# Performance work log

Hardware: AMD Instinct MI355X
Metric: run time of the kernel (lower is better)

Reference implementation:

```python
import jax, jax.numpy as jnp
import numpy as np

D_MODEL = 1024
N_HEAD = 16
B, S = 4, 2048


def setup_inputs() -> dict:
    key = jax.random.key(0)
    ks = jax.random.split(key, 13)
    s = 1.0 / np.sqrt(D_MODEL)
    inp = {
        "query": jax.random.normal(ks[0], (B, S, D_MODEL), jnp.float32),
        "key_": jax.random.normal(ks[1], (B, S, D_MODEL), jnp.float32),
        "value": jax.random.normal(ks[2], (B, S, D_MODEL), jnp.float32),
        "mask": jax.random.randint(ks[3], (B, 1, S, S), 0, 2, jnp.int32),
        "Wq": jax.random.normal(ks[4], (D_MODEL, D_MODEL), jnp.float32) * s,
        "bq": jax.random.normal(ks[5], (D_MODEL,), jnp.float32) * 0.02,
        "Wk": jax.random.normal(ks[6], (D_MODEL, D_MODEL), jnp.float32) * s,
        "bk": jax.random.normal(ks[7], (D_MODEL,), jnp.float32) * 0.02,
        "Wv": jax.random.normal(ks[8], (D_MODEL, D_MODEL), jnp.float32) * s,
        "bv": jax.random.normal(ks[9], (D_MODEL,), jnp.float32) * 0.02,
        "Wo": jax.random.normal(ks[10], (D_MODEL, D_MODEL), jnp.float32) * s,
        "bo": jax.random.normal(ks[11], (D_MODEL,), jnp.float32) * 0.02,
    }
    return inp


def _split_heads(x):
    b, l, d = x.shape
    return x.reshape(b, l, N_HEAD, d // N_HEAD).transpose(0, 2, 1, 3)  # [B,H,S,Dh]


def reference(query, key_, value, mask, Wq, bq, Wk, bk, Wv, bv, Wo, bo):
    q = _split_heads(query @ Wq + bq)
    k = _split_heads(key_ @ Wk + bk)
    v = _split_heads(value @ Wv + bv)
    dh = q.shape[-1]
    score = jnp.einsum("bhqd,bhkd->bhqk", q, k) / jnp.sqrt(jnp.float32(dh))
    score = jnp.where(mask == 0, jnp.float32(-1e9), score)
    attn = jax.nn.softmax(score, axis=-1)
    out = jnp.einsum("bhqk,bhkd->bhqd", attn, v)  # [B,H,S,Dh]
    b, h, l, d = out.shape
    out = out.transpose(0, 2, 1, 3).reshape(b, l, h * d)
    return out @ Wo + bo
```

## Files before the change

### kernel.cpp

```cpp
#include <hip/hip_runtime.h>
#include <hip/hip_bf16.h>
#include <stdint.h>

#define D_MODEL 1024
#define NHEAD   16
#define DH      64
#define BATCH   4
#define SEQ     2048

typedef __bf16 bf16;
typedef __bf16 bf16x8 __attribute__((ext_vector_type(8)));
typedef __bf16 bf16x4 __attribute__((ext_vector_type(4)));
typedef float  f32x4  __attribute__((ext_vector_type(4)));

#define QSCALE 0.180336876f
#define MFIX   24.0f

__device__ __forceinline__ void gload16(const void* g, void* l) {
    __builtin_amdgcn_global_load_lds((const __attribute__((address_space(1))) uint32_t*)g,
                                     (__attribute__((address_space(3))) uint32_t*)l, 16, 0, 0);
}

__global__ __launch_bounds__(256) void wt4_kernel(const float* __restrict__ W0,
                                                  const float* __restrict__ W1,
                                                  const float* __restrict__ W2,
                                                  const float* __restrict__ W3,
                                                  bf16* __restrict__ Wt3,
                                                  bf16* __restrict__ WtO) {
    __shared__ float t[32][33];
    int z = blockIdx.z;
    const float* W = z == 0 ? W0 : (z == 1 ? W1 : (z == 2 ? W2 : W3));
    bf16* Wt = z < 3 ? Wt3 + (long long)z * (1024ll * 1024) : WtO;
    int x = threadIdx.x, y = threadIdx.y;
    int bi = blockIdx.x * 32;
    int bj = blockIdx.y * 32;
#pragma unroll
    for (int j = 0; j < 4; ++j)
        t[y + j * 8][x] = W[(bi + y + j * 8) * D_MODEL + bj + x];
    __syncthreads();
#pragma unroll
    for (int j = 0; j < 4; ++j)
        Wt[(long long)(bj + y + j * 8) * D_MODEL + bi + x] = (bf16)t[x][y + j * 8];
}

__global__ __launch_bounds__(256) void f2b3_kernel(const float* __restrict__ q,
                                                   const float* __restrict__ k,
                                                   const float* __restrict__ v,
                                                   bf16* __restrict__ out) {
    int third = blockIdx.x >> 12;
    int wi = blockIdx.x & 4095;
    const float* in = third == 0 ? q : (third == 1 ? k : v);
    long long i = (long long)wi * 2048 + threadIdx.x * 8;
    float4 a = *(const float4*)&in[i];
    float4 b = *(const float4*)&in[i + 4];
    bf16x8 o;
    o[0] = (bf16)a.x; o[1] = (bf16)a.y; o[2] = (bf16)a.z; o[3] = (bf16)a.w;
    o[4] = (bf16)b.x; o[5] = (bf16)b.y; o[6] = (bf16)b.z; o[7] = (bf16)b.w;
    *(bf16x8*)&out[(long long)third * (8192ll * 1024) + i] = o;
}

__global__ __launch_bounds__(256) void maskpack_kernel(const int* __restrict__ mask,
                                                       unsigned* __restrict__ bits) {
    long long tid = (long long)blockIdx.x * 256 + threadIdx.x;
    int lane = threadIdx.x & 63;
    long long wid = tid >> 6;
    int m = mask[wid * 64 + lane];
    unsigned long long bal = __ballot(m != 0);
    if (lane == 0) *(unsigned long long*)&bits[wid * 2] = bal;
}

__global__ __launch_bounds__(256) void gemm_qkv_kernel(const bf16* __restrict__ A3,
                                                       const bf16* __restrict__ Wt3,
                                                       const float* __restrict__ bq,
                                                       const float* __restrict__ bk,
                                                       const float* __restrict__ bv,
                                                       bf16* __restrict__ out3) {
    constexpr int K = D_MODEL;
    __shared__ bf16 As[2][128][32];
    __shared__ bf16 Bs[2][128][32];
    int tid = threadIdx.x;
    int l = tid & 63, w = tid >> 6;
    int g = l >> 4, c = l & 15;
    int wm = (w >> 1) * 64, wn = (w & 1) * 64;
    int third = blockIdx.y >> 6;
    long long m0 = (long long)(blockIdx.y & 63) * 128;
    int n0 = blockIdx.x * 128;
    const bf16* A  = A3  + (long long)third * (8192ll * 1024);
    const bf16* Bt = Wt3 + (long long)third * (1024ll * 1024);
    const float* bias = third == 0 ? bq : (third == 1 ? bk : bv);
    float osc = third == 0 ? QSCALE : 1.0f;
    bf16* C = out3 + (long long)third * (8192ll * 1024);
    int srow = l >> 2, scolb = (l & 3) * 16;

    f32x4 acc[4][4] = {};

    for (int k0 = 0; k0 < K; k0 += 64) {
#pragma unroll
        for (int kk = 0; kk < 2; ++kk)
#pragma unroll
            for (int i = 0; i < 2; ++i) {
                int ck = w * 2 + i;
                int row = ck * 16 + srow;
                gload16((const char*)(A + (m0 + row) * K + k0 + kk * 32) + scolb,
                        (char*)&As[kk][0][0] + ck * 1024);
                gload16((const char*)(Bt + (long long)(n0 + row) * K + k0 + kk * 32) + scolb,
                        (char*)&Bs[kk][0][0] + ck * 1024);
            }
        __syncthreads();
#pragma unroll
        for (int kk = 0; kk < 2; ++kk) {
            bf16x8 af[4], bfr[4];
#pragma unroll
            for (int i = 0; i < 4; ++i) af[i] = *(const bf16x8*)&As[kk][wm + i * 16 + c][g * 8];
#pragma unroll
            for (int i = 0; i < 4; ++i) bfr[i] = *(const bf16x8*)&Bs[kk][wn + i * 16 + c][g * 8];
#pragma unroll
            for (int mi = 0; mi < 4; ++mi)
#pragma unroll
                for (int ni = 0; ni < 4; ++ni)
                    acc[mi][ni] = __builtin_amdgcn_mfma_f32_16x16x32_bf16(af[mi], bfr[ni],
                                                                         acc[mi][ni], 0, 0, 0);
        }
        __syncthreads();
    }

#pragma unroll
    for (int mi = 0; mi < 4; ++mi) {
#pragma unroll
        for (int ni = 0; ni < 4; ++ni) {
            int n = n0 + wn + ni * 16 + c;
            float bv_ = bias[n];
            int h = n >> 6, f = n & 63;
#pragma unroll
            for (int r = 0; r < 4; ++r) {
                long long m = m0 + wm + mi * 16 + g * 4 + r;
                float val = (acc[mi][ni][r] + bv_) * osc;
                int b = (int)(m >> 11), s = (int)(m & 2047);
                C[((long long)(b * NHEAD + h) * SEQ + s) * DH + f] = (bf16)val;
            }
        }
    }
}

__global__ __launch_bounds__(256) void gemm_out_kernel(const bf16* __restrict__ A,
                                                       const bf16* __restrict__ Bt,
                                                       const float* __restrict__ bias,
                                                       float* __restrict__ Cptr) {
    constexpr int K = D_MODEL;
    __shared__ bf16 As[2][128][32];
    __shared__ bf16 Bs[2][128][32];
    int tid = threadIdx.x;
    int l = tid & 63, w = tid >> 6;
    int g = l >> 4, c = l & 15;
    int wm = (w >> 1) * 64, wn = (w & 1) * 64;
    long long m0 = (long long)blockIdx.y * 128;
    int n0 = blockIdx.x * 128;
    int srow = l >> 2, scolb = (l & 3) * 16;

    f32x4 acc[4][4] = {};

    for (int k0 = 0; k0 < K; k0 += 64) {
#pragma unroll
        for (int kk = 0; kk < 2; ++kk)
#pragma unroll
            for (int i = 0; i < 2; ++i) {
                int ck = w * 2 + i;
                int row = ck * 16 + srow;
                gload16((const char*)(A + (m0 + row) * K + k0 + kk * 32) + scolb,
                        (char*)&As[kk][0][0] + ck * 1024);
                gload16((const char*)(Bt + (long long)(n0 + row) * K + k0 + kk * 32) + scolb,
                        (char*)&Bs[kk][0][0] + ck * 1024);
            }
        __syncthreads();
#pragma unroll
        for (int kk = 0; kk < 2; ++kk) {
            bf16x8 af[4], bfr[4];
#pragma unroll
            for (int i = 0; i < 4; ++i) af[i] = *(const bf16x8*)&As[kk][wm + i * 16 + c][g * 8];
#pragma unroll
            for (int i = 0; i < 4; ++i) bfr[i] = *(const bf16x8*)&Bs[kk][wn + i * 16 + c][g * 8];
#pragma unroll
            for (int mi = 0; mi < 4; ++mi)
#pragma unroll
                for (int ni = 0; ni < 4; ++ni)
                    acc[mi][ni] = __builtin_amdgcn_mfma_f32_16x16x32_bf16(af[mi], bfr[ni],
                                                                         acc[mi][ni], 0, 0, 0);
        }
        __syncthreads();
    }

#pragma unroll
    for (int mi = 0; mi < 4; ++mi)
#pragma unroll
        for (int ni = 0; ni < 4; ++ni) {
            int n = n0 + wn + ni * 16 + c;
            float bv = bias[n];
#pragma unroll
            for (int r = 0; r < 4; ++r) {
                long long m = m0 + wm + mi * 16 + g * 4 + r;
                Cptr[m * D_MODEL + n] = acc[mi][ni][r] + bv;
            }
        }
}

__global__ __launch_bounds__(256) void vtrans_kernel(const bf16* __restrict__ in,
                                                     bf16* __restrict__ out) {
    __shared__ bf16 t[64][72];
    int bh = blockIdx.y;
    int s0 = blockIdx.x * 64;
    int tid = threadIdx.x;
#pragma unroll
    for (int i = 0; i < 2; ++i) {
        int ck = tid + i * 256;
        int s = ck >> 3, f0 = (ck & 7) * 8;
        bf16x8 v = *(const bf16x8*)&in[((long long)bh * SEQ + s0 + s) * DH + f0];
#pragma unroll
        for (int j = 0; j < 8; ++j) t[f0 + j][s] = v[j];
    }
    __syncthreads();
#pragma unroll
    for (int i = 0; i < 2; ++i) {
        int ck = tid + i * 256;
        int f = ck >> 3, c0 = (ck & 7) * 8;
        bf16x8 v = *(const bf16x8*)&t[f][c0];
        *(bf16x8*)&out[((long long)bh * DH + f) * SEQ + s0 + c0] = v;
    }
}

__global__ __launch_bounds__(512) void attn_kernel(const bf16* __restrict__ Q,
                                                   const bf16* __restrict__ Kt,
                                                   const bf16* __restrict__ Vt,
                                                   const unsigned* __restrict__ bits,
                                                   bf16* __restrict__ O) {
    __shared__ bf16 Ks[2][64][64];
    __shared__ bf16 Vs[2][64][64];
    __shared__ bf16 Ps[8][16][64];
    int tid = threadIdx.x;
    int l = tid & 63, w = tid >> 6;
    int g = l >> 4, c = l & 15;
    int orig = blockIdx.x;
    int swz = (orig & 7) * 128 + (orig >> 3);
    int bh = swz >> 4, qb = swz & 15;
    int b = bh >> 4, h = bh & 15;
    int q0 = qb * 128;
    int q = q0 + w * 16 + c;

    const long long kbase = (long long)bh * SEQ * DH;
    const long long vbase = (long long)bh * DH * SEQ;

    bf16x8 qf0, qf1;
    {
        long long base = ((long long)bh * SEQ + q) * DH + g * 8;
        qf0 = *(const bf16x8*)&Q[base];
        qf1 = *(const bf16x8*)&Q[base + 32];
    }

    int row = tid >> 3;
    int scolb = ((tid & 7) ^ (row & 7)) * 16;

    f32x4 o_acc[4] = {};
    float lsum = 0.f;
    const unsigned* mrow = &bits[((long long)b * SEQ + q) * (SEQ / 32)];
    int gx8 = (g ^ (c & 7)) * 8;

    auto stage = [&](int buf, int kv0) {
        gload16((const char*)(Kt + kbase + (long long)(kv0 + row) * DH) + scolb,
                (char*)&Ks[buf][0][0] + w * 1024);
        gload16((const char*)(Vt + vbase + (long long)row * SEQ + kv0) + scolb,
                (char*)&Vs[buf][0][0] + w * 1024);
    };
    stage(0, 0);

    int cur = 0;
    for (int t = 0; t < SEQ / 64; ++t) {
        __syncthreads();
        if (t + 1 < SEQ / 64) stage(cur ^ 1, (t + 1) * 64);

        f32x4 sacc[4] = {};
#pragma unroll
        for (int nb = 0; nb < 4; ++nb) {
            bf16x8 k0f = *(const bf16x8*)&Ks[cur][nb * 16 + c][gx8];
            bf16x8 k1f = *(const bf16x8*)&Ks[cur][nb * 16 + c][gx8 ^ 32];
            sacc[nb] = __builtin_amdgcn_mfma_f32_16x16x32_bf16(k0f, qf0, sacc[nb], 0, 0, 0);
            sacc[nb] = __builtin_amdgcn_mfma_f32_16x16x32_bf16(k1f, qf1, sacc[nb], 0, 0, 0);
        }

        uint2 mb = *(const uint2*)&mrow[t * 2];
        unsigned wsel[4] = { mb.x >> (g * 4), mb.x >> (16 + g * 4),
                             mb.y >> (g * 4), mb.y >> (16 + g * 4) };
#pragma unroll
        for (int nb = 0; nb < 4; ++nb) {
            bf16x4 pk;
#pragma unroll
            for (int r = 0; r < 4; ++r) {
                float p = exp2f(sacc[nb][r] - MFIX);
                p = ((wsel[nb] >> r) & 1u) ? p : 0.f;
                lsum += p;
                pk[r] = (bf16)p;
            }
            *(bf16x4*)&Ps[w][c][(nb * 16 + g * 4) ^ ((c & 7) * 8)] = pk;
        }

#pragma unroll
        for (int kvb = 0; kvb < 2; ++kvb) {
            bf16x8 pf = *(const bf16x8*)&Ps[w][c][((kvb * 4 + g) ^ (c & 7)) * 8];
#pragma unroll
            for (int fb = 0; fb < 4; ++fb) {
                bf16x8 vf = *(const bf16x8*)&Vs[cur][fb * 16 + c][((kvb * 4 + g) ^ (c & 7)) * 8];
                o_acc[fb] = __builtin_amdgcn_mfma_f32_16x16x32_bf16(pf, vf, o_acc[fb], 0, 0, 0);
            }
        }
        cur ^= 1;
    }

    lsum += __shfl_xor(lsum, 16);
    lsum += __shfl_xor(lsum, 32);

    float linv[4];
#pragma unroll
    for (int r = 0; r < 4; ++r) linv[r] = 1.0f / __shfl(lsum, g * 4 + r);
#pragma unroll
    for (int fb = 0; fb < 4; ++fb)
#pragma unroll
        for (int r = 0; r < 4; ++r) {
            int qq = q0 + w * 16 + g * 4 + r;
            O[((long long)b * SEQ + qq) * D_MODEL + h * DH + fb * 16 + c] =
                (bf16)(o_acc[fb][r] * linv[r]);
        }
}

extern "C" void kernel_launch(void* const* d_in, const int* in_sizes, int n_in,
                              void* d_out, int out_size, void* d_ws, size_t ws_size,
                              hipStream_t stream) {
    const float* query = (const float*)d_in[0];
    const float* key_  = (const float*)d_in[1];
    const float* value = (const float*)d_in[2];
    const int*   mask  = (const int*)d_in[3];
    const float* Wq = (const float*)d_in[4];
    const float* bq = (const float*)d_in[5];
    const float* Wk = (const float*)d_in[6];
    const float* bk = (const float*)d_in[7];
    const float* Wv = (const float*)d_in[8];
    const float* bv = (const float*)d_in[9];
    const float* Wo = (const float*)d_in[10];
    const float* bo = (const float*)d_in[11];
    float* out = (float*)d_out;

    char* ws = (char*)d_ws;
    bf16* A3    = (bf16*)(ws);
    bf16* V16t  = (bf16*)(ws);
    bf16* O16   = (bf16*)(ws + (16ll << 20));
    bf16* Q16   = (bf16*)(ws + (48ll << 20));
    bf16* K16   = (bf16*)(ws + (64ll << 20));
    bf16* V16   = (bf16*)(ws + (80ll << 20));
    bf16* Wt3   = (bf16*)(ws + (96ll << 20));
    bf16* WtO   = (bf16*)(ws + (102ll << 20));
    unsigned* bits = (unsigned*)(ws + (104ll << 20));

    wt4_kernel<<<dim3(32, 32, 4), dim3(32, 8), 0, stream>>>(Wq, Wk, Wv, Wo, Wt3, WtO);

    maskpack_kernel<<<65536, 256, 0, stream>>>(mask, bits);

    f2b3_kernel<<<12288, 256, 0, stream>>>(query, key_, value, A3);

    gemm_qkv_kernel<<<dim3(8, 192), 256, 0, stream>>>(A3, Wt3, bq, bk, bv, Q16);

    vtrans_kernel<<<dim3(32, 64), 256, 0, stream>>>(V16, V16t);

    attn_kernel<<<1024, 512, 0, stream>>>(Q16, K16, V16t, bits, O16);

    gemm_out_kernel<<<dim3(8, 64), 256, 0, stream>>>(O16, WtO, bo, out);
}
```

Baseline: 467.0 us.

## Load K and V fragments directly from global into registers, dropping LDS staging

Replaces the LDS double-buffered K/V staging with per-wave direct global loads into register fragments. K is ping-ponged between two register sets so the next tile's K load overlaps the current tile's compute, and the per-tile block-wide __syncthreads is removed. Each of the 8 waves now fetches the same K/V tiles separately, so global/L2 traffic rises eightfold. Register pressure also grows, and it is paired with a launch-bounds occupancy hint of 4 blocks.

```diff
diff --git a/kernel.cpp b/kernel.cpp
--- a/kernel.cpp
+++ b/kernel.cpp
@@ -227,13 +227,11 @@
     }
 }
 
-__global__ __launch_bounds__(512) void attn_kernel(const bf16* __restrict__ Q,
-                                                   const bf16* __restrict__ Kt,
-                                                   const bf16* __restrict__ Vt,
-                                                   const unsigned* __restrict__ bits,
-                                                   bf16* __restrict__ O) {
-    __shared__ bf16 Ks[2][64][64];
-    __shared__ bf16 Vs[2][64][64];
+__global__ __launch_bounds__(512, 4) void attn_kernel(const bf16* __restrict__ Q,
+                                                      const bf16* __restrict__ Kt,
+                                                      const bf16* __restrict__ Vt,
+                                                      const unsigned* __restrict__ bits,
+                                                      bf16* __restrict__ O) {
     __shared__ bf16 Ps[8][16][64];
     int tid = threadIdx.x;
     int l = tid & 63, w = tid >> 6;
@@ -245,8 +243,8 @@
     int q0 = qb * 128;
     int q = q0 + w * 16 + c;
 
-    const long long kbase = (long long)bh * SEQ * DH;
-    const long long vbase = (long long)bh * DH * SEQ;
+    const bf16* Kp = Kt + (long long)bh * SEQ * DH;
+    const bf16* Vp = Vt + (long long)bh * DH * SEQ;
 
     bf16x8 qf0, qf1;
     {
@@ -255,36 +253,36 @@
         qf1 = *(const bf16x8*)&Q[base + 32];
     }
 
-    int row = tid >> 3;
-    int scolb = ((tid & 7) ^ (row & 7)) * 16;
-
     f32x4 o_acc[4] = {};
     float lsum = 0.f;
     const unsigned* mrow = &bits[((long long)b * SEQ + q) * (SEQ / 32)];
-    int gx8 = (g ^ (c & 7)) * 8;
-
-    auto stage = [&](int buf, int kv0) {
-        gload16((const char*)(Kt + kbase + (long long)(kv0 + row) * DH) + scolb,
-                (char*)&Ks[buf][0][0] + w * 1024);
-        gload16((const char*)(Vt + vbase + (long long)row * SEQ + kv0) + scolb,
-                (char*)&Vs[buf][0][0] + w * 1024);
+    int pswz = (c & 7) * 8;
+
+    bf16x8 kA[4][2], kB[4][2], vf[4][2];
+
+    auto loadK = [&](bf16x8 (&kf)[4][2], int kv0) {
+#pragma unroll
+        for (int nb = 0; nb < 4; ++nb) {
+            const bf16* p = Kp + (kv0 + nb * 16 + c) * DH + g * 8;
+            kf[nb][0] = *(const bf16x8*)p;
+            kf[nb][1] = *(const bf16x8*)(p + 32);
+        }
     };
-    stage(0, 0);
-
-    int cur = 0;
-    for (int t = 0; t < SEQ / 64; ++t) {
-        __syncthreads();
-        if (t + 1 < SEQ / 64) stage(cur ^ 1, (t + 1) * 64);
-
+    auto loadV = [&](int kv0) {
+#pragma unroll
+        for (int fb = 0; fb < 4; ++fb) {
+            const bf16* p = Vp + (fb * 16 + c) * SEQ + kv0 + g * 8;
+            vf[fb][0] = *(const bf16x8*)p;
+            vf[fb][1] = *(const bf16x8*)(p + 32);
+        }
+    };
+    auto compute = [&](bf16x8 (&kf)[4][2], int t) {
         f32x4 sacc[4] = {};
 #pragma unroll
         for (int nb = 0; nb < 4; ++nb) {
-            bf16x8 k0f = *(const bf16x8*)&Ks[cur][nb * 16 + c][gx8];
-            bf16x8 k1f = *(const bf16x8*)&Ks[cur][nb * 16 + c][gx8 ^ 32];
-            sacc[nb] = __builtin_amdgcn_mfma_f32_16x16x32_bf16(k0f, qf0, sacc[nb], 0, 0, 0);
-            sacc[nb] = __builtin_amdgcn_mfma_f32_16x16x32_bf16(k1f, qf1, sacc[nb], 0, 0, 0);
-        }
-
+            sacc[nb] = __builtin_amdgcn_mfma_f32_16x16x32_bf16(kf[nb][0], qf0, sacc[nb], 0, 0, 0);
+            sacc[nb] = __builtin_amdgcn_mfma_f32_16x16x32_bf16(kf[nb][1], qf1, sacc[nb], 0, 0, 0);
+        }
         uint2 mb = *(const uint2*)&mrow[t * 2];
         unsigned wsel[4] = { mb.x >> (g * 4), mb.x >> (16 + g * 4),
                              mb.y >> (g * 4), mb.y >> (16 + g * 4) };
@@ -298,19 +296,27 @@
                 lsum += p;
                 pk[r] = (bf16)p;
             }
-            *(bf16x4*)&Ps[w][c][(nb * 16 + g * 4) ^ ((c & 7) * 8)] = pk;
-        }
-
+            *(bf16x4*)&Ps[w][c][(nb * 16 + g * 4) ^ pswz] = pk;
+        }
 #pragma unroll
         for (int kvb = 0; kvb < 2; ++kvb) {
             bf16x8 pf = *(const bf16x8*)&Ps[w][c][((kvb * 4 + g) ^ (c & 7)) * 8];
 #pragma unroll
-            for (int fb = 0; fb < 4; ++fb) {
-                bf16x8 vf = *(const bf16x8*)&Vs[cur][fb * 16 + c][((kvb * 4 + g) ^ (c & 7)) * 8];
-                o_acc[fb] = __builtin_amdgcn_mfma_f32_16x16x32_bf16(pf, vf, o_acc[fb], 0, 0, 0);
-            }
-        }
-        cur ^= 1;
+            for (int fb = 0; fb < 4; ++fb)
+                o_acc[fb] = __builtin_amdgcn_mfma_f32_16x16x32_bf16(pf, vf[fb][kvb],
+                                                                    o_acc[fb], 0, 0, 0);
+        }
+    };
+
+    constexpr int NT = SEQ / 64;
+    loadK(kA, 0);
+    for (int t = 0; t < NT; t += 2) {
+        loadV(t * 64);
+        loadK(kB, (t + 1) * 64);
+        compute(kA, t);
+        loadV((t + 1) * 64);
+        if (t + 2 < NT) loadK(kA, (t + 2) * 64);
+        compute(kB, t + 1);
     }
 
     lsum += __shfl_xor(lsum, 16);
```

Result: slower. 938.9 us (+101.0%).
